# Optimization experiments

Hardware: AMD Instinct MI355X
Metric: run time of the kernel (lower is better)

## Reference

```python
import jax, jax.numpy as jnp
import numpy as np

N = 50000
DEG = 16
E = N * DEG
IN_F, HID, OUT_F = 512, 128, 64
SLOPE = 0.2


def setup_inputs() -> dict:
    key = jax.random.key(0)
    ks = jax.random.split(key, 10)
    row_ptr = jnp.arange(N + 1, dtype=jnp.int64) * DEG          # uniform-degree CSR
    col_idx = jax.random.randint(ks[0], (E,), 0, N, dtype=jnp.int64)
    x = jax.random.normal(ks[1], (N, IN_F), dtype=jnp.float32)
    s1 = 1.0 / np.sqrt(IN_F)
    s2 = 1.0 / np.sqrt(HID)
    return {
        "row_ptr": row_ptr,
        "col_idx": col_idx,
        "input_feature": x,
        "W1": jax.random.normal(ks[2], (IN_F, HID), dtype=jnp.float32) * s1,
        "attn_l1": jax.random.normal(ks[3], (HID,), dtype=jnp.float32) * s2,
        "attn_r1": jax.random.normal(ks[4], (HID,), dtype=jnp.float32) * s2,
        "bias1": jnp.zeros((HID,), dtype=jnp.float32),
        "W2": jax.random.normal(ks[5], (HID, OUT_F), dtype=jnp.float32) * s2,
        "attn_l2": jax.random.normal(ks[6], (OUT_F,), dtype=jnp.float32) * 0.125,
        "attn_r2": jax.random.normal(ks[7], (OUT_F,), dtype=jnp.float32) * 0.125,
        "bias2": jnp.zeros((OUT_F,), dtype=jnp.float32),
    }


def gat_layer(row_ptr, col_idx, x, W, attn_l, attn_r, bias):
    n = row_ptr.shape[0] - 1
    e = col_idx.shape[0]
    h = x @ W                                   # [N, F] dense GEMM
    el = h @ attn_l                             # [N] dst attention term
    er = h @ attn_r                             # [N] src attention term
    # edge -> destination row via CSR row_ptr
    dst = jnp.searchsorted(row_ptr, jnp.arange(e, dtype=row_ptr.dtype), side="right") - 1
    src = col_idx
    score = jax.nn.leaky_relu(el[dst] + er[src], negative_slope=SLOPE)  # [E]
    # neighborhood softmax over edges sharing a destination
    smax = jax.ops.segment_max(score, dst, num_segments=n)
    ex = jnp.exp(score - smax[dst])
    ssum = jax.ops.segment_sum(ex, dst, num_segments=n)
    alpha = ex / ssum[dst]                      # [E]
    # weighted gather-scatter aggregation
    out = jax.ops.segment_sum(alpha[:, None] * h[src], dst, num_segments=n)
    return out + bias


def reference(row_ptr, col_idx, input_feature, W1, attn_l1, attn_r1, bias1,
              W2, attn_l2, attn_r2, bias2):
    x = gat_layer(row_ptr, col_idx, input_feature, W1, attn_l1, attn_r1, bias1)
    x = gat_layer(row_ptr, col_idx, x, W2, attn_l2, attn_r2, bias2)
    return x
```

## Files before the change

### kernel.cpp

```cpp
#include <hip/hip_runtime.h>
#include <hip/hip_bf16.h>

#define Nn 50000
#define DEG 16
#define IN_F 512
#define HID 128
#define OUT_F 64
#define SLOPE 0.2f

typedef __attribute__((ext_vector_type(8))) short bf16x8;
typedef __attribute__((ext_vector_type(4))) float f32x4;

__device__ __forceinline__ unsigned short f2bf(float f) {
    return __builtin_bit_cast(unsigned short, __float2bfloat16(f));
}
__device__ __forceinline__ float bf2f(unsigned short u) {
    return __bfloat162float(__builtin_bit_cast(__hip_bfloat16, u));
}

__global__ void __launch_bounds__(256) prep_kernel(
        const float* __restrict__ W1, const float* __restrict__ W2,
        const int* __restrict__ row_ptr,
        unsigned short* __restrict__ w1t, unsigned short* __restrict__ w2t,
        int* __restrict__ flag64) {
    int g = blockIdx.x * 256 + threadIdx.x;
    if (g == 0) {
        *flag64 = (row_ptr[1] == DEG) ? 0 : 1;
    }
    if (g < IN_F * HID) {
        int k = g >> 7, c = g & 127;
        w1t[c * IN_F + k] = f2bf(W1[g]);
    } else {
        int g2 = g - IN_F * HID;
        if (g2 < HID * OUT_F) {
            int k = g2 >> 6, c = g2 & 63;
            w2t[c * HID + k] = f2bf(W2[g2]);
        }
    }
}

template<int K, int F, bool A_BF16>
__global__ void __launch_bounds__(256) gemm_reg(
        const void* __restrict__ Ain, const unsigned short* __restrict__ WT,
        const float* __restrict__ alv, const float* __restrict__ arv,
        unsigned short* __restrict__ Hb, float* __restrict__ el,
        float* __restrict__ er, int M) {
    constexpr int NT = F / 16;
    const int tid  = threadIdx.x;
    const int lane = tid & 63;
    const int w    = tid >> 6;
    const int ln   = lane & 15, q = lane >> 4;
    const int mb   = blockIdx.x * 128 + w * 32;

    int m0 = mb + ln;      if (m0 > M - 1) m0 = M - 1;
    int m1 = mb + 16 + ln; if (m1 > M - 1) m1 = M - 1;

    f32x4 acc[2][NT] = {};
    const unsigned short* bb = WT + (size_t)ln * K;

    #pragma unroll
    for (int ks = 0; ks < K / 32; ++ks) {
        const int kk = ks * 32 + q * 8;
        bf16x8 af0, af1;
        if constexpr (A_BF16) {
            const unsigned short* Ab = (const unsigned short*)Ain;
            af0 = *(const bf16x8*)&Ab[(size_t)m0 * K + kk];
            af1 = *(const bf16x8*)&Ab[(size_t)m1 * K + kk];
        } else {
            const float* Af = (const float*)Ain;
            f32x4 va0 = *(const f32x4*)&Af[(size_t)m0 * K + kk];
            f32x4 va1 = *(const f32x4*)&Af[(size_t)m0 * K + kk + 4];
            f32x4 vb0 = *(const f32x4*)&Af[(size_t)m1 * K + kk];
            f32x4 vb1 = *(const f32x4*)&Af[(size_t)m1 * K + kk + 4];
            #pragma unroll
            for (int jj = 0; jj < 4; ++jj) {
                af0[jj]     = (short)f2bf(va0[jj]);
                af0[jj + 4] = (short)f2bf(va1[jj]);
                af1[jj]     = (short)f2bf(vb0[jj]);
                af1[jj + 4] = (short)f2bf(vb1[jj]);
            }
        }
        #pragma unroll
        for (int nt = 0; nt < NT; ++nt) {
            bf16x8 bfr = *(const bf16x8*)&bb[(size_t)nt * 16 * K + kk];
            acc[0][nt] = __builtin_amdgcn_mfma_f32_16x16x32_bf16(af0, bfr, acc[0][nt], 0, 0, 0);
            acc[1][nt] = __builtin_amdgcn_mfma_f32_16x16x32_bf16(af1, bfr, acc[1][nt], 0, 0, 0);
        }
    }

    float av[NT], bv[NT];
    #pragma unroll
    for (int nt = 0; nt < NT; ++nt) {
        av[nt] = alv[nt * 16 + ln];
        bv[nt] = arv[nt * 16 + ln];
    }
    #pragma unroll
    for (int fr = 0; fr < 2; ++fr) {
        #pragma unroll
        for (int r = 0; r < 4; ++r) {
            float sl = 0.f, sr = 0.f;
            #pragma unroll
            for (int nt = 0; nt < NT; ++nt) {
                float v = acc[fr][nt][r];
                sl += v * av[nt];
                sr += v * bv[nt];
            }
            #pragma unroll
            for (int m = 1; m < 16; m <<= 1) {
                sl += __shfl_xor(sl, m);
                sr += __shfl_xor(sr, m);
            }
            int grow = mb + fr * 16 + q * 4 + r;
            if (grow < M) {
                #pragma unroll
                for (int nt = 0; nt < NT; ++nt)
                    Hb[(size_t)grow * F + nt * 16 + ln] = f2bf(acc[fr][nt][r]);
                if (ln == 0) { el[grow] = sl; er[grow] = sr; }
            }
        }
    }
}

__global__ void __launch_bounds__(256) agg1_k(
        const int* __restrict__ col, const int* __restrict__ flag64,
        const float* __restrict__ el, const float* __restrict__ er,
        const unsigned short* __restrict__ Hb, const float* __restrict__ bias,
        unsigned short* __restrict__ Ob) {
    int lane = threadIdx.x & 63;
    int node = blockIdx.x * 4 + (threadIdx.x >> 6);
    int j    = lane & 15;
    int e    = node * DEG + j;
    int src  = (*flag64) ? (int)((const long long*)col)[e] : col[e];
    float sc = el[node] + er[src];
    sc = sc >= 0.f ? sc : SLOPE * sc;
    float mx = sc;
    #pragma unroll
    for (int m = 1; m < 16; m <<= 1) mx = fmaxf(mx, __shfl_xor(mx, m));
    float ex = __expf(sc - mx);
    float sm = ex;
    #pragma unroll
    for (int m = 1; m < 16; m <<= 1) sm += __shfl_xor(sm, m);
    float alpha = ex / sm;

    float a0 = 0.f, a1 = 0.f;
    #pragma unroll
    for (int jj = 0; jj < DEG; ++jj) {
        int   sj = __shfl(src, jj, 16);
        float aj = __shfl(alpha, jj, 16);
        unsigned int hv = *(const unsigned int*)&Hb[(size_t)sj * HID + lane * 2];
        a0 += aj * bf2f((unsigned short)(hv & 0xffffu));
        a1 += aj * bf2f((unsigned short)(hv >> 16));
    }
    a0 += bias[lane * 2];
    a1 += bias[lane * 2 + 1];
    unsigned int pk = (unsigned int)f2bf(a0) | ((unsigned int)f2bf(a1) << 16);
    *(unsigned int*)&Ob[(size_t)node * HID + lane * 2] = pk;
}

__global__ void __launch_bounds__(256) agg2_k(
        const int* __restrict__ col, const int* __restrict__ flag64,
        const float* __restrict__ el, const float* __restrict__ er,
        const unsigned short* __restrict__ Hb, const float* __restrict__ bias,
        float* __restrict__ out) {
    int lane = threadIdx.x & 63;
    int node = blockIdx.x * 4 + (threadIdx.x >> 6);
    int j    = lane & 15;
    int e    = node * DEG + j;
    int src  = (*flag64) ? (int)((const long long*)col)[e] : col[e];
    float sc = el[node] + er[src];
    sc = sc >= 0.f ? sc : SLOPE * sc;
    float mx = sc;
    #pragma unroll
    for (int m = 1; m < 16; m <<= 1) mx = fmaxf(mx, __shfl_xor(mx, m));
    float ex = __expf(sc - mx);
    float sm = ex;
    #pragma unroll
    for (int m = 1; m < 16; m <<= 1) sm += __shfl_xor(sm, m);
    float alpha = ex / sm;

    float a0 = 0.f;
    #pragma unroll
    for (int jj = 0; jj < DEG; ++jj) {
        int   sj = __shfl(src, jj, 16);
        float aj = __shfl(alpha, jj, 16);
        a0 += aj * bf2f(Hb[(size_t)sj * OUT_F + lane]);
    }
    out[(size_t)node * OUT_F + lane] = a0 + bias[lane];
}

extern "C" void kernel_launch(void* const* d_in, const int* in_sizes, int n_in,
                              void* d_out, int out_size, void* d_ws, size_t ws_size,
                              hipStream_t stream) {
    const int*   row_ptr = (const int*)d_in[0];
    const int*   col_idx = (const int*)d_in[1];
    const float* x   = (const float*)d_in[2];
    const float* W1  = (const float*)d_in[3];
    const float* al1 = (const float*)d_in[4];
    const float* ar1 = (const float*)d_in[5];
    const float* b1  = (const float*)d_in[6];
    const float* W2  = (const float*)d_in[7];
    const float* al2 = (const float*)d_in[8];
    const float* ar2 = (const float*)d_in[9];
    const float* b2  = (const float*)d_in[10];
    float* out = (float*)d_out;

    float* ws = (float*)d_ws;
    unsigned short* h1b = (unsigned short*)ws;
    unsigned short* o1b = (unsigned short*)(ws + 3200000);
    unsigned short* h2b = (unsigned short*)(ws + 6400000);
    float* el1 = ws + 8000000;
    float* er1 = ws + 8050000;
    float* el2 = ws + 8100000;
    float* er2 = ws + 8150000;
    unsigned short* w1t = (unsigned short*)(ws + 8200000);
    unsigned short* w2t = (unsigned short*)(ws + 8232768);
    int* flag64 = (int*)(ws + 8236864);

    prep_kernel<<<(IN_F * HID + HID * OUT_F + 255) / 256, 256, 0, stream>>>(
        W1, W2, row_ptr, w1t, w2t, flag64);

    gemm_reg<512, 128, false><<<(Nn + 127) / 128, 256, 0, stream>>>(
        x, w1t, al1, ar1, h1b, el1, er1, Nn);
    agg1_k<<<Nn / 4, 256, 0, stream>>>(col_idx, flag64, el1, er1, h1b, b1, o1b);

    gemm_reg<128, 64, true><<<(Nn + 127) / 128, 256, 0, stream>>>(
        o1b, w2t, al2, ar2, h2b, el2, er2, Nn);
    agg2_k<<<Nn / 4, 256, 0, stream>>>(col_idx, flag64, el2, er2, h2b, b2, out);
}
```

Measured before the change: 256.5 us.

## Fuse layer-1 aggregation with layer-2 GEMM and shrink GEMM1 row tile

The layer-1 aggregation now writes each 16-node block's aggregated features into shared memory and runs the layer-2 GEMM (plus el2/er2 attention dots) in the same kernel. This removes the o1b intermediate buffer round trip and one kernel launch. Separately, the first GEMM now handles 16 rows per wave instead of 32, giving twice as many blocks but less reuse of the W1 fragments per MFMA.

```diff
diff --git a/kernel.cpp b/kernel.cpp
--- a/kernel.cpp
+++ b/kernel.cpp
@@ -39,9 +39,9 @@
     }
 }
 
-template<int K, int F, bool A_BF16>
-__global__ void __launch_bounds__(256) gemm_reg(
-        const void* __restrict__ Ain, const unsigned short* __restrict__ WT,
+template<int K, int F>
+__global__ void __launch_bounds__(256) gemm1_reg(
+        const float* __restrict__ Af, const unsigned short* __restrict__ WT,
         const float* __restrict__ alv, const float* __restrict__ arv,
         unsigned short* __restrict__ Hb, float* __restrict__ el,
         float* __restrict__ er, int M) {
@@ -50,41 +50,28 @@
     const int lane = tid & 63;
     const int w    = tid >> 6;
     const int ln   = lane & 15, q = lane >> 4;
-    const int mb   = blockIdx.x * 128 + w * 32;
-
-    int m0 = mb + ln;      if (m0 > M - 1) m0 = M - 1;
-    int m1 = mb + 16 + ln; if (m1 > M - 1) m1 = M - 1;
-
-    f32x4 acc[2][NT] = {};
-    const unsigned short* bb = WT + (size_t)ln * K;
+    const int mb   = blockIdx.x * 64 + w * 16;
+
+    int m0 = mb + ln; if (m0 > M - 1) m0 = M - 1;
+    const float* a0p = Af + (size_t)m0 * K;
+
+    f32x4 acc[NT] = {};
 
     #pragma unroll
     for (int ks = 0; ks < K / 32; ++ks) {
         const int kk = ks * 32 + q * 8;
-        bf16x8 af0, af1;
-        if constexpr (A_BF16) {
-            const unsigned short* Ab = (const unsigned short*)Ain;
-            af0 = *(const bf16x8*)&Ab[(size_t)m0 * K + kk];
-            af1 = *(const bf16x8*)&Ab[(size_t)m1 * K + kk];
-        } else {
-            const float* Af = (const float*)Ain;
-            f32x4 va0 = *(const f32x4*)&Af[(size_t)m0 * K + kk];
-            f32x4 va1 = *(const f32x4*)&Af[(size_t)m0 * K + kk + 4];
-            f32x4 vb0 = *(const f32x4*)&Af[(size_t)m1 * K + kk];
-            f32x4 vb1 = *(const f32x4*)&Af[(size_t)m1 * K + kk + 4];
-            #pragma unroll
-            for (int jj = 0; jj < 4; ++jj) {
-                af0[jj]     = (short)f2bf(va0[jj]);
-                af0[jj + 4] = (short)f2bf(va1[jj]);
-                af1[jj]     = (short)f2bf(vb0[jj]);
-                af1[jj + 4] = (short)f2bf(vb1[jj]);
-            }
+        f32x4 va0 = *(const f32x4*)(a0p + kk);
+        f32x4 va1 = *(const f32x4*)(a0p + kk + 4);
+        bf16x8 af;
+        #pragma unroll
+        for (int jj = 0; jj < 4; ++jj) {
+            af[jj]     = (short)f2bf(va0[jj]);
+            af[jj + 4] = (short)f2bf(va1[jj]);
         }
         #pragma unroll
         for (int nt = 0; nt < NT; ++nt) {
-            bf16x8 bfr = *(const bf16x8*)&bb[(size_t)nt * 16 * K + kk];
-            acc[0][nt] = __builtin_amdgcn_mfma_f32_16x16x32_bf16(af0, bfr, acc[0][nt], 0, 0, 0);
-            acc[1][nt] = __builtin_amdgcn_mfma_f32_16x16x32_bf16(af1, bfr, acc[1][nt], 0, 0, 0);
+            bf16x8 bfr = *(const bf16x8*)&WT[(size_t)(nt * 16 + ln) * K + kk];
+            acc[nt] = __builtin_amdgcn_mfma_f32_16x16x32_bf16(af, bfr, acc[nt], 0, 0, 0);
         }
     }
 
@@ -95,66 +82,110 @@
         bv[nt] = arv[nt * 16 + ln];
     }
     #pragma unroll
-    for (int fr = 0; fr < 2; ++fr) {
-        #pragma unroll
-        for (int r = 0; r < 4; ++r) {
-            float sl = 0.f, sr = 0.f;
+    for (int r = 0; r < 4; ++r) {
+        float sl = 0.f, sr = 0.f;
+        #pragma unroll
+        for (int nt = 0; nt < NT; ++nt) {
+            float v = acc[nt][r];
+            sl += v * av[nt];
+            sr += v * bv[nt];
+        }
+        #pragma unroll
+        for (int m = 1; m < 16; m <<= 1) {
+            sl += __shfl_xor(sl, m);
+            sr += __shfl_xor(sr, m);
+        }
+        int grow = mb + q * 4 + r;
+        if (grow < M) {
             #pragma unroll
-            for (int nt = 0; nt < NT; ++nt) {
-                float v = acc[fr][nt][r];
-                sl += v * av[nt];
-                sr += v * bv[nt];
-            }
-            #pragma unroll
-            for (int m = 1; m < 16; m <<= 1) {
-                sl += __shfl_xor(sl, m);
-                sr += __shfl_xor(sr, m);
-            }
-            int grow = mb + fr * 16 + q * 4 + r;
-            if (grow < M) {
-                #pragma unroll
-                for (int nt = 0; nt < NT; ++nt)
-                    Hb[(size_t)grow * F + nt * 16 + ln] = f2bf(acc[fr][nt][r]);
-                if (ln == 0) { el[grow] = sl; er[grow] = sr; }
-            }
-        }
-    }
-}
-
-__global__ void __launch_bounds__(256) agg1_k(
+            for (int nt = 0; nt < NT; ++nt)
+                Hb[(size_t)grow * F + nt * 16 + ln] = f2bf(acc[nt][r]);
+            if (ln == 0) { el[grow] = sl; er[grow] = sr; }
+        }
+    }
+}
+
+__global__ void __launch_bounds__(256) fused_agg_gemm2(
         const int* __restrict__ col, const int* __restrict__ flag64,
-        const float* __restrict__ el, const float* __restrict__ er,
-        const unsigned short* __restrict__ Hb, const float* __restrict__ bias,
-        unsigned short* __restrict__ Ob) {
-    int lane = threadIdx.x & 63;
-    int node = blockIdx.x * 4 + (threadIdx.x >> 6);
-    int j    = lane & 15;
-    int e    = node * DEG + j;
-    int src  = (*flag64) ? (int)((const long long*)col)[e] : col[e];
-    float sc = el[node] + er[src];
-    sc = sc >= 0.f ? sc : SLOPE * sc;
-    float mx = sc;
-    #pragma unroll
-    for (int m = 1; m < 16; m <<= 1) mx = fmaxf(mx, __shfl_xor(mx, m));
-    float ex = __expf(sc - mx);
-    float sm = ex;
-    #pragma unroll
-    for (int m = 1; m < 16; m <<= 1) sm += __shfl_xor(sm, m);
-    float alpha = ex / sm;
-
-    float a0 = 0.f, a1 = 0.f;
-    #pragma unroll
-    for (int jj = 0; jj < DEG; ++jj) {
-        int   sj = __shfl(src, jj, 16);
-        float aj = __shfl(alpha, jj, 16);
-        unsigned int hv = *(const unsigned int*)&Hb[(size_t)sj * HID + lane * 2];
-        a0 += aj * bf2f((unsigned short)(hv & 0xffffu));
-        a1 += aj * bf2f((unsigned short)(hv >> 16));
-    }
-    a0 += bias[lane * 2];
-    a1 += bias[lane * 2 + 1];
-    unsigned int pk = (unsigned int)f2bf(a0) | ((unsigned int)f2bf(a1) << 16);
-    *(unsigned int*)&Ob[(size_t)node * HID + lane * 2] = pk;
+        const float* __restrict__ el1, const float* __restrict__ er1,
+        const unsigned short* __restrict__ Hb, const float* __restrict__ b1,
+        const unsigned short* __restrict__ w2t,
+        const float* __restrict__ al2, const float* __restrict__ ar2,
+        unsigned short* __restrict__ H2, float* __restrict__ el2,
+        float* __restrict__ er2) {
+    constexpr int STR = 136;
+    __shared__ unsigned short at[16 * STR];
+    __shared__ float redl[16][4];
+    __shared__ float redr[16][4];
+
+    const int tid  = threadIdx.x;
+    const int lane = tid & 63;
+    const int w    = tid >> 6;
+    const int ln   = lane & 15, q = lane >> 4;
+    const int nb   = blockIdx.x * 16;
+    const int use64 = *flag64;
+
+    #pragma unroll
+    for (int n = 0; n < 4; ++n) {
+        int node = nb + w * 4 + n;
+        int j    = lane & 15;
+        int e    = node * DEG + j;
+        int src  = use64 ? (int)((const long long*)col)[e] : col[e];
+        float sc = el1[node] + er1[src];
+        sc = sc >= 0.f ? sc : SLOPE * sc;
+        float mx = sc;
+        #pragma unroll
+        for (int m = 1; m < 16; m <<= 1) mx = fmaxf(mx, __shfl_xor(mx, m));
+        float ex = __expf(sc - mx);
+        float sm = ex;
+        #pragma unroll
+        for (int m = 1; m < 16; m <<= 1) sm += __shfl_xor(sm, m);
+        float alpha = ex / sm;
+
+        float a0 = 0.f, a1 = 0.f;
+        #pragma unroll
+        for (int jj = 0; jj < DEG; ++jj) {
+            int   sj = __shfl(src, jj, 16);
+            float aj = __shfl(alpha, jj, 16);
+            unsigned int hv = *(const unsigned int*)&Hb[(size_t)sj * HID + lane * 2];
+            a0 += aj * bf2f((unsigned short)(hv & 0xffffu));
+            a1 += aj * bf2f((unsigned short)(hv >> 16));
+        }
+        a0 += b1[lane * 2];
+        a1 += b1[lane * 2 + 1];
+        unsigned int pk = (unsigned int)f2bf(a0) | ((unsigned int)f2bf(a1) << 16);
+        *(unsigned int*)&at[(w * 4 + n) * STR + lane * 2] = pk;
+    }
+    __syncthreads();
+
+    f32x4 acc = {};
+    const unsigned short* bb = w2t + (size_t)(w * 16 + ln) * HID;
+    #pragma unroll
+    for (int ks = 0; ks < HID / 32; ++ks) {
+        bf16x8 af  = *(const bf16x8*)&at[ln * STR + ks * 32 + q * 8];
+        bf16x8 bfr = *(const bf16x8*)&bb[ks * 32 + q * 8];
+        acc = __builtin_amdgcn_mfma_f32_16x16x32_bf16(af, bfr, acc, 0, 0, 0);
+    }
+
+    float av = al2[w * 16 + ln], bv = ar2[w * 16 + ln];
+    #pragma unroll
+    for (int r = 0; r < 4; ++r) {
+        float v  = acc[r];
+        float sl = v * av, sr = v * bv;
+        #pragma unroll
+        for (int m = 1; m < 16; m <<= 1) {
+            sl += __shfl_xor(sl, m);
+            sr += __shfl_xor(sr, m);
+        }
+        int rowl = q * 4 + r;
+        H2[(size_t)(nb + rowl) * OUT_F + w * 16 + ln] = f2bf(v);
+        if (ln == 0) { redl[rowl][w] = sl; redr[rowl][w] = sr; }
+    }
+    __syncthreads();
+    if (tid < 16) {
+        el2[nb + tid] = redl[tid][0] + redl[tid][1] + redl[tid][2] + redl[tid][3];
+        er2[nb + tid] = redr[tid][0] + redr[tid][1] + redr[tid][2] + redr[tid][3];
+    }
 }
 
 __global__ void __launch_bounds__(256) agg2_k(
@@ -206,24 +237,23 @@
 
     float* ws = (float*)d_ws;
     unsigned short* h1b = (unsigned short*)ws;
-    unsigned short* o1b = (unsigned short*)(ws + 3200000);
-    unsigned short* h2b = (unsigned short*)(ws + 6400000);
-    float* el1 = ws + 8000000;
-    float* er1 = ws + 8050000;
-    float* el2 = ws + 8100000;
-    float* er2 = ws + 8150000;
-    unsigned short* w1t = (unsigned short*)(ws + 8200000);
-    unsigned short* w2t = (unsigned short*)(ws + 8232768);
-    int* flag64 = (int*)(ws + 8236864);
+    unsigned short* h2b = (unsigned short*)(ws + 3200000);
+    float* el1 = ws + 5000000;
+    float* er1 = ws + 5050000;
+    float* el2 = ws + 5100000;
+    float* er2 = ws + 5150000;
+    unsigned short* w1t = (unsigned short*)(ws + 5200000);
+    unsigned short* w2t = (unsigned short*)(ws + 5232768);
+    int* flag64 = (int*)(ws + 5236864);
 
     prep_kernel<<<(IN_F * HID + HID * OUT_F + 255) / 256, 256, 0, stream>>>(
         W1, W2, row_ptr, w1t, w2t, flag64);
 
-    gemm_reg<512, 128, false><<<(Nn + 127) / 128, 256, 0, stream>>>(
+    gemm1_reg<512, 128><<<(Nn + 63) / 64, 256, 0, stream>>>(
         x, w1t, al1, ar1, h1b, el1, er1, Nn);
-    agg1_k<<<Nn / 4, 256, 0, stream>>>(col_idx, flag64, el1, er1, h1b, b1, o1b);
-
-    gemm_reg<128, 64, true><<<(Nn + 127) / 128, 256, 0, stream>>>(
-        o1b, w2t, al2, ar2, h2b, el2, er2, Nn);
+
+    fused_agg_gemm2<<<Nn / 16, 256, 0, stream>>>(
+        col_idx, flag64, el1, er1, h1b, b1, w2t, al2, ar2, h2b, el2, er2);
+
     agg2_k<<<Nn / 4, 256, 0, stream>>>(col_idx, flag64, el2, er2, h2b, b2, out);
 }
```

Measured after the change: 278.7 us. 1.09x slower.
